# Kernel tuning notes

Measured on AMD Instinct MI355X. Metric: run time of the kernel, lower is better.

## Reference

```python
import jax, jax.numpy as jnp
import numpy as np

N_NODES = 50000
N_EDGES = 800000
IN_F, HID_F, OUT_F = 256, 128, 64


def setup_inputs() -> dict:
    key = jax.random.key(0)
    ks = jax.random.split(key, 9)
    glorot = lambda k, shp: jax.random.normal(k, shp, jnp.float32) * np.sqrt(2.0 / (shp[0] + shp[1]))
    return {
        "x": jax.random.normal(ks[0], (N_NODES, IN_F), jnp.float32),
        "W1": glorot(ks[1], (IN_F, HID_F)),
        "b1": jnp.zeros((HID_F,), jnp.float32),
        "W2": glorot(ks[2], (HID_F, OUT_F)),
        "b2": jnp.zeros((OUT_F,), jnp.float32),
        "Wf": glorot(ks[3], (OUT_F, 2)),
        "bf": jnp.zeros((2,), jnp.float32),
        "src": jax.random.randint(ks[4], (N_EDGES,), 0, N_NODES, jnp.int32),
        "dst": jax.random.randint(ks[5], (N_EDGES,), 0, N_NODES, jnp.int32),
    }


def _gcn_layer(x, src, dst, W, b):
    # DGL GraphConv, norm='both': h = D_in^{-1/2} A D_out^{-1/2} (x W) + b
    n = x.shape[0]
    ones = jnp.ones((src.shape[0],), x.dtype)
    deg_out = jnp.clip(jax.ops.segment_sum(ones, src, num_segments=n), 1.0)
    deg_in = jnp.clip(jax.ops.segment_sum(ones, dst, num_segments=n), 1.0)
    h = x @ W  # transform first (in_feats >= out_feats), cheaper messages
    h = h * jax.lax.rsqrt(deg_out)[:, None]
    agg = jax.ops.segment_sum(h[src], dst, num_segments=n)  # [N, F] sparse aggregate
    return agg * jax.lax.rsqrt(deg_in)[:, None] + b


def reference(x, W1, b1, W2, b2, Wf, bf, src, dst):
    h1 = jax.nn.relu(_gcn_layer(x, src, dst, W1, b1))
    hidden = _gcn_layer(h1, src, dst, W2, b2)
    logits = hidden @ Wf + bf
    return (logits, hidden)
```

## Files before the change

### kernel.cpp

```cpp
#include <hip/hip_runtime.h>
#include <hip/hip_bf16.h>
#include <cstdint>
#include <cstddef>

#define NNODES 50000
#define NEDGES 800000
#define NCH    256
#define CHUNK1 3136
#define NBUCK  196
#define GB1    782
#define SHB    64
#define SHE    12500
#define SHEV   (SHE / 1024)
#define PBN    256
#define PBR    196

typedef unsigned short u16;
typedef unsigned int u32;
typedef short bfrag8 __attribute__((ext_vector_type(8)));
typedef float f32x4 __attribute__((ext_vector_type(4)));

__device__ __forceinline__ u16 f2bf(float f) {
    union { float f; uint32_t i; } v; v.f = f;
    uint32_t r = (v.i + 0x7FFFu + ((v.i >> 16) & 1u)) >> 16;
    return (u16)r;
}
__device__ __forceinline__ float bflo(u32 p) { union { uint32_t i; float f; } v; v.i = p << 16; return v.f; }
__device__ __forceinline__ float bfhi(u32 p) { union { uint32_t i; float f; } v; v.i = p & 0xFFFF0000u; return v.f; }

__global__ __launch_bounds__(256) void pre_kernel(const float* __restrict__ W1, const float* __restrict__ W2,
                                                  u16* __restrict__ P1, u16* __restrict__ P2,
                                                  const int* __restrict__ src, const int* __restrict__ dst,
                                                  u32* __restrict__ histS, u32* __restrict__ histD,
                                                  u16* __restrict__ gh1, int nE) {
    __shared__ u32 hh[12500];
    int b = blockIdx.x, t = threadIdx.x;
    if (b < 2 * SHB) {
        const int* col = (b < SHB) ? src : dst;
        int bb = (b < SHB) ? b : b - SHB;
        for (int j = t; j < 12500; j += 256) hh[j] = 0;
        __syncthreads();
        int beg = bb * SHE;
        const uint4* col4 = (const uint4*)(col + beg);
        #pragma unroll 4
        for (int k = 0; k < SHEV; k++) {
            uint4 e = col4[k * 256 + t];
            atomicAdd(&hh[e.x >> 2], 1u << ((e.x & 3) * 8));
            atomicAdd(&hh[e.y >> 2], 1u << ((e.y & 3) * 8));
            atomicAdd(&hh[e.z >> 2], 1u << ((e.z & 3) * 8));
            atomicAdd(&hh[e.w >> 2], 1u << ((e.w & 3) * 8));
        }
        for (int i = beg + SHEV * 1024 + t; i < beg + SHE; i += 256) {
            u32 n = (u32)col[i];
            atomicAdd(&hh[n >> 2], 1u << ((n & 3) * 8));
        }
        __syncthreads();
        u32* out = ((b < SHB) ? histS : histD) + (size_t)bb * 12500;
        for (int j = t; j < 12500; j += 256) out[j] = hh[j];
    } else if (b < 2 * SHB + NCH) {
        int c = b - 2 * SHB;
        hh[t] = 0;
        __syncthreads();
        int beg = c * CHUNK1, end = min(beg + CHUNK1, nE);
        const uint4* d4 = (const uint4*)(dst + beg);
        int n4 = (end - beg) >> 2;
        for (int k = t; k < n4; k += 256) {
            uint4 e = d4[k];
            atomicAdd(&hh[e.x >> 8], 1u);
            atomicAdd(&hh[e.y >> 8], 1u);
            atomicAdd(&hh[e.z >> 8], 1u);
            atomicAdd(&hh[e.w >> 8], 1u);
        }
        __syncthreads();
        gh1[c * NCH + t] = (u16)hh[t];
    } else {
        int i = (b - 2 * SHB - NCH) * 256 + t;
        if (i < 256 * 128) {
            int k = i >> 7, n = i & 127;
            P1[((((k >> 3) << 7) + n) << 3) | (k & 7)] = f2bf(W1[i]);
        }
        if (i < 128 * 64) {
            int k = i >> 6, n = i & 63;
            P2[((((k >> 3) << 6) + n) << 3) | (k & 7)] = f2bf(W2[i]);
        }
    }
}

__global__ __launch_bounds__(256) void scat_deg(const int* __restrict__ src, const int* __restrict__ dst,
                                                const u16* __restrict__ gh1,
                                                const u32* __restrict__ histS, const u32* __restrict__ histD,
                                                int* __restrict__ deg_out, int* __restrict__ deg_in,
                                                int* __restrict__ gdh, int* __restrict__ part1,
                                                u32* __restrict__ sbuf, int nE) {
    int t = threadIdx.x, c = blockIdx.x;
    __shared__ int sd[256];
    __shared__ u32 base[256];
    __shared__ u32 lh[256];
    __shared__ int cnt64[64];
    if (t < 64) cnt64[t] = 0;
    int tot = 0, par = 0;
    #pragma unroll 8
    for (int cc = 0; cc < NCH; cc++) {
        int v = (int)gh1[cc * NCH + t];
        tot += v;
        par += (cc < c) ? v : 0;
    }
    if (c == 0) part1[t] = tot;
    sd[t] = tot;
    __syncthreads();
    #pragma unroll
    for (int o = 1; o < 256; o <<= 1) {
        int add = (t >= o) ? sd[t - o] : 0;
        __syncthreads();
        sd[t] += add;
        __syncthreads();
    }
    base[t] = (u32)((sd[t] - tot) + par);
    lh[t] = 0;
    __syncthreads();
    int beg = c * CHUNK1, end = min(beg + CHUNK1, nE);
    const uint4* s4 = (const uint4*)(src + beg);
    const uint4* d4 = (const uint4*)(dst + beg);
    int n4 = (end - beg) >> 2;
    for (int k = t; k < n4; k += 256) {
        uint4 es = s4[k], ed = d4[k];
        u32 el, dg, r;
        el = (ed.x << 16) | es.x; dg = el >> 24; r = atomicAdd(&lh[dg], 1); sbuf[base[dg] + r] = el;
        el = (ed.y << 16) | es.y; dg = el >> 24; r = atomicAdd(&lh[dg], 1); sbuf[base[dg] + r] = el;
        el = (ed.z << 16) | es.z; dg = el >> 24; r = atomicAdd(&lh[dg], 1); sbuf[base[dg] + r] = el;
        el = (ed.w << 16) | es.w; dg = el >> 24; r = atomicAdd(&lh[dg], 1); sbuf[base[dg] + r] = el;
    }
    int n = c * PBR + t;
    if (t < PBR && n < NNODES) {
        int w = n >> 2, sh = (n & 3) * 8;
        int so = 0, si = 0;
        #pragma unroll 8
        for (int r = 0; r < SHB; r++) {
            so += (int)((histS[(size_t)r * 12500 + w] >> sh) & 255u);
            si += (int)((histD[(size_t)r * 12500 + w] >> sh) & 255u);
        }
        deg_out[n] = so;
        deg_in[n] = si;
        atomicAdd(&cnt64[si > 63 ? 63 : si], 1);
    }
    __syncthreads();
    if (t < 64) gdh[c * 64 + t] = cnt64[t];
}

template <int K, int N, bool AF32>
__device__ __forceinline__ void gemm_body(const void* __restrict__ A_, const u16* __restrict__ Wp,
                                          const int* __restrict__ deg, u16* __restrict__ out, int M, int bx) {
    const int lane = threadIdx.x & 63;
    const int wave = threadIdx.x >> 6;
    const int m = lane & 15;
    const int q = lane >> 4;
    const int row0 = bx * 64 + wave * 16;

    int rowa = row0 + m; if (rowa > M - 1) rowa = M - 1;

    constexpr int NT = N / 16;
    f32x4 acc[NT];
    #pragma unroll
    for (int t = 0; t < NT; t++) acc[t] = (f32x4){0.f, 0.f, 0.f, 0.f};

    #pragma unroll
    for (int kc = 0; kc < K; kc += 32) {
        bfrag8 af;
        if constexpr (AF32) {
            const float* ap = (const float*)A_ + (size_t)rowa * K + q * 8 + kc;
            const float4 x0 = *(const float4*)(ap);
            const float4 x1 = *(const float4*)(ap + 4);
            af[0] = (short)f2bf(x0.x); af[1] = (short)f2bf(x0.y);
            af[2] = (short)f2bf(x0.z); af[3] = (short)f2bf(x0.w);
            af[4] = (short)f2bf(x1.x); af[5] = (short)f2bf(x1.y);
            af[6] = (short)f2bf(x1.z); af[7] = (short)f2bf(x1.w);
        } else {
            const u16* ap = (const u16*)A_ + (size_t)rowa * K + q * 8 + kc;
            af = *(const bfrag8*)ap;
        }
        const u16* bbase = Wp + ((size_t)(((kc >> 3) + q) * N) + m) * 8;
        #pragma unroll
        for (int t = 0; t < NT; t++) {
            bfrag8 bf_ = *(const bfrag8*)(bbase + t * 128);
            acc[t] = __builtin_amdgcn_mfma_f32_16x16x32_bf16(af, bf_, acc[t], 0, 0, 0);
        }
    }
    #pragma unroll
    for (int r = 0; r < 4; r++) {
        int gr = row0 + q * 4 + r;
        if (gr < M) {
            int dO = deg[gr]; if (dO < 1) dO = 1;
            float s = rsqrtf((float)dO);
            #pragma unroll
            for (int t = 0; t < NT; t++)
                out[(size_t)gr * N + t * 16 + m] = f2bf(acc[t][r] * s);
        }
    }
}

__global__ __launch_bounds__(256) void sort_gemm(const u32* __restrict__ sbuf, const int* __restrict__ part1,
                                                 u32* __restrict__ sorted, int* __restrict__ rp,
                                                 const float* __restrict__ x, const u16* __restrict__ Wp1,
                                                 const int* __restrict__ deg_out, const int* __restrict__ deg_in,
                                                 const int* __restrict__ gdh, int* __restrict__ perm,
                                                 u16* __restrict__ h, int nE) {
    int b = blockIdx.x, t = threadIdx.x;
    if (b < NBUCK) {
        __shared__ int sd[256];
        __shared__ int cnt[256];
        __shared__ int cursor[256];
        int v = part1[t];
        sd[t] = v;
        __syncthreads();
        #pragma unroll
        for (int o = 1; o < 256; o <<= 1) {
            int add = (t >= o) ? sd[t - o] : 0;
            __syncthreads();
            sd[t] += add;
            __syncthreads();
        }
        __shared__ int bs_s, bl_s;
        if (t == b) { bs_s = sd[t] - v; bl_s = v; }
        __syncthreads();
        int bstart = bs_s, bend = bstart + bl_s;
        cnt[t] = 0;
        __syncthreads();
        for (int i = bstart + t; i < bend; i += 256)
            atomicAdd(&cnt[(sbuf[i] >> 16) & 255u], 1);
        __syncthreads();
        int cv = cnt[t];
        sd[t] = cv;
        __syncthreads();
        #pragma unroll
        for (int o = 1; o < 256; o <<= 1) {
            int add = (t >= o) ? sd[t - o] : 0;
            __syncthreads();
            sd[t] += add;
            __syncthreads();
        }
        int excl = sd[t] - cv;
        int node = b * 256 + t;
        if (node < NNODES) rp[node] = bstart + excl;
        if (b == NBUCK - 1 && t == 0) rp[NNODES] = nE;
        cursor[t] = excl;
        __syncthreads();
        for (int i = bstart + t; i < bend; i += 256) {
            u32 el = sbuf[i];
            int r = atomicAdd(&cursor[(el >> 16) & 255u], 1);
            sorted[bstart + r] = el;
        }
    } else if (b < NBUCK + GB1) {
        gemm_body<256, 128, true>(x, Wp1, deg_out, h, NNODES, b - NBUCK);
    } else {
        int pb = b - NBUCK - GB1;
        __shared__ int cse[64];
        __shared__ int cur[64];
        if (t < 64) {
            int s_all = 0, s_pre = 0;
            for (int q2 = 0; q2 < PBN; q2++) {
                int v = gdh[q2 * 64 + t];
                s_all += v;
                s_pre += (q2 < pb) ? v : 0;
            }
            cse[t] = s_all;
            cur[t] = s_pre;
        }
        __syncthreads();
        if (t == 0) {
            int s = 0;
            for (int d2 = 0; d2 < 64; d2++) { int v = cse[d2]; cse[d2] = s; s += v; }
        }
        __syncthreads();
        if (t < 64) cur[t] += cse[t];
        __syncthreads();
        int n = pb * PBR + t;
        if (t < PBR && n < NNODES) {
            int d = deg_in[n]; d = d > 63 ? 63 : d;
            int p = atomicAdd(&cur[d], 1);
            perm[p] = n;
        }
    }
}

__global__ __launch_bounds__(256) void gather1f(const uint4* __restrict__ h, const int* __restrict__ row_ptr,
                                                const u32* __restrict__ sorted, const float* __restrict__ b1,
                                                const int* __restrict__ perm, const int* __restrict__ deg_out,
                                                const u16* __restrict__ Wp2, u16* __restrict__ h2) {
    __shared__ __align__(16) u16 sh[16 * 136];
    int t = threadIdx.x;
    int qw = t >> 4;
    int l = t & 15;
    int g = blockIdx.x * 16 + qw;
    int node = perm[g];
    int beg = row_ptr[node], end = row_ptr[node + 1];
    float a[8] = {0.f, 0.f, 0.f, 0.f, 0.f, 0.f, 0.f, 0.f};
    for (int e = beg; e < end; e += 8) {
        uint4 p[8];
        #pragma unroll
        for (int j = 0; j < 8; j++) {
            int ee = e + j; ee = (ee < end - 1) ? ee : end - 1;
            p[j] = h[(size_t)(sorted[ee] & 0xFFFFu) * 16 + l];
        }
        #pragma unroll
        for (int j = 0; j < 8; j++)
            if (e + j < end) {
                a[0] += bflo(p[j].x); a[1] += bfhi(p[j].x);
                a[2] += bflo(p[j].y); a[3] += bfhi(p[j].y);
                a[4] += bflo(p[j].z); a[5] += bfhi(p[j].z);
                a[6] += bflo(p[j].w); a[7] += bfhi(p[j].w);
            }
    }
    int dI = end - beg; if (dI < 1) dI = 1;
    float r = rsqrtf((float)dI);
    const float4 bA = *(const float4*)(b1 + 8 * l);
    const float4 bB = *(const float4*)(b1 + 8 * l + 4);
    float v0 = fmaxf(a[0] * r + bA.x, 0.f), v1 = fmaxf(a[1] * r + bA.y, 0.f);
    float v2 = fmaxf(a[2] * r + bA.z, 0.f), v3 = fmaxf(a[3] * r + bA.w, 0.f);
    float v4 = fmaxf(a[4] * r + bB.x, 0.f), v5 = fmaxf(a[5] * r + bB.y, 0.f);
    float v6 = fmaxf(a[6] * r + bB.z, 0.f), v7 = fmaxf(a[7] * r + bB.w, 0.f);
    uint4 o;
    o.x = ((u32)f2bf(v1) << 16) | f2bf(v0);
    o.y = ((u32)f2bf(v3) << 16) | f2bf(v2);
    o.z = ((u32)f2bf(v5) << 16) | f2bf(v4);
    o.w = ((u32)f2bf(v7) << 16) | f2bf(v6);
    *(uint4*)&sh[qw * 136 + l * 8] = o;
    __syncthreads();
    const int lane = t & 63;
    const int m = lane & 15;
    const int q = lane >> 4;
    const int w = t >> 6;
    f32x4 acc = (f32x4){0.f, 0.f, 0.f, 0.f};
    #pragma unroll
    for (int kc = 0; kc < 128; kc += 32) {
        bfrag8 af = *(const bfrag8*)&sh[m * 136 + q * 8 + kc];
        bfrag8 bf_ = *(const bfrag8*)(Wp2 + ((size_t)(((kc >> 3) + q) * 64) + w * 16 + m) * 8);
        acc = __builtin_amdgcn_mfma_f32_16x16x32_bf16(af, bf_, acc, 0, 0, 0);
    }
    #pragma unroll
    for (int rr = 0; rr < 4; rr++) {
        int li = q * 4 + rr;
        int nd = perm[blockIdx.x * 16 + li];
        int dO = deg_out[nd]; if (dO < 1) dO = 1;
        float s = rsqrtf((float)dO);
        h2[(size_t)nd * 64 + w * 16 + m] = f2bf(acc[rr] * s);
    }
}

__global__ __launch_bounds__(256) void gather2(const uint4* __restrict__ h2, const int* __restrict__ row_ptr,
                                               const u32* __restrict__ sorted, const float* __restrict__ b2,
                                               const float* __restrict__ Wf, const float* __restrict__ bfv,
                                               const int* __restrict__ perm,
                                               float* __restrict__ logits, float* __restrict__ hidden, int nNodes) {
    int g = (blockIdx.x * 256 + threadIdx.x) >> 3;
    int l = threadIdx.x & 7;
    if (g >= nNodes) return;
    int node = perm[g];
    int beg = row_ptr[node], end = row_ptr[node + 1];
    float a[8] = {0.f, 0.f, 0.f, 0.f, 0.f, 0.f, 0.f, 0.f};
    for (int e = beg; e < end; e += 8) {
        uint4 p[8];
        #pragma unroll
        for (int j = 0; j < 8; j++) {
            int ee = e + j; ee = (ee < end - 1) ? ee : end - 1;
            p[j] = h2[(size_t)(sorted[ee] & 0xFFFFu) * 8 + l];
        }
        #pragma unroll
        for (int j = 0; j < 8; j++)
            if (e + j < end) {
                a[0] += bflo(p[j].x); a[1] += bfhi(p[j].x);
                a[2] += bflo(p[j].y); a[3] += bfhi(p[j].y);
                a[4] += bflo(p[j].z); a[5] += bfhi(p[j].z);
                a[6] += bflo(p[j].w); a[7] += bfhi(p[j].w);
            }
    }
    int dI = end - beg; if (dI < 1) dI = 1;
    float r = rsqrtf((float)dI);
    float v[8];
    #pragma unroll
    for (int f = 0; f < 8; f++) v[f] = a[f] * r + b2[8 * l + f];
    float4 oA = {v[0], v[1], v[2], v[3]};
    float4 oB = {v[4], v[5], v[6], v[7]};
    ((float4*)hidden)[(size_t)node * 16 + 2 * l + 0] = oA;
    ((float4*)hidden)[(size_t)node * 16 + 2 * l + 1] = oB;
    float l0 = 0.f, l1 = 0.f;
    #pragma unroll
    for (int f = 0; f < 8; f++) {
        l0 += v[f] * Wf[(8 * l + f) * 2 + 0];
        l1 += v[f] * Wf[(8 * l + f) * 2 + 1];
    }
    #pragma unroll
    for (int off = 4; off > 0; off >>= 1) {
        l0 += __shfl_down(l0, off, 8);
        l1 += __shfl_down(l1, off, 8);
    }
    if (l == 0) {
        logits[(size_t)node * 2 + 0] = l0 + bfv[0];
        logits[(size_t)node * 2 + 1] = l1 + bfv[1];
    }
}

extern "C" void kernel_launch(void* const* d_in, const int* in_sizes, int n_in,
                              void* d_out, int out_size, void* d_ws, size_t ws_size,
                              hipStream_t stream) {
    const float* x   = (const float*)d_in[0];
    const float* W1  = (const float*)d_in[1];
    const float* b1  = (const float*)d_in[2];
    const float* W2  = (const float*)d_in[3];
    const float* b2  = (const float*)d_in[4];
    const float* Wf  = (const float*)d_in[5];
    const float* bfv = (const float*)d_in[6];
    const int* src = (const int*)d_in[7];
    const int* dst = (const int*)d_in[8];

    float* out_logits = (float*)d_out;
    float* out_hidden = (float*)d_out + 2 * NNODES;

    char* ws = (char*)d_ws;
    size_t off = 0;
    auto alloc = [&](size_t bytes) { void* p = ws + off; off += (bytes + 255) & ~(size_t)255; return p; };
    u16*   gh1     = (u16*)alloc(NCH * NCH * 2);
    int*   part1   = (int*)alloc(256 * 4);
    u32*   sbuf    = (u32*)alloc((size_t)NEDGES * 4);
    u32*   sorted  = (u32*)alloc((size_t)NEDGES * 4);
    u32*   histS   = (u32*)alloc((size_t)SHB * 12500 * 4);
    u32*   histD   = (u32*)alloc((size_t)SHB * 12500 * 4);
    int*   deg     = (int*)alloc(2 * NNODES * 4);
    int*   row_ptr = (int*)alloc((NNODES + 1) * 4);
    int*   gdh     = (int*)alloc(PBN * 64 * 4);
    int*   perm    = (int*)alloc(NNODES * 4);
    u16*   Wp1     = (u16*)alloc(256 * 128 * 2);
    u16*   Wp2     = (u16*)alloc(128 * 64 * 2);
    u16*   h       = (u16*)alloc((size_t)NNODES * 128 * 2);
    u16*   h2      = (u16*)alloc((size_t)NNODES * 64 * 2);

    int* deg_out = deg;
    int* deg_in  = deg + NNODES;

    pre_kernel<<<2 * SHB + NCH + 128, 256, 0, stream>>>(W1, W2, Wp1, Wp2, src, dst, histS, histD, gh1, NEDGES);
    scat_deg<<<NCH, 256, 0, stream>>>(src, dst, gh1, histS, histD, deg_out, deg_in, gdh, part1, sbuf, NEDGES);
    sort_gemm<<<NBUCK + GB1 + PBN, 256, 0, stream>>>(sbuf, part1, sorted, row_ptr, x, Wp1,
                                                     deg_out, deg_in, gdh, perm, h, NEDGES);
    gather1f<<<NNODES / 16, 256, 0, stream>>>((const uint4*)h, row_ptr, sorted, b1, perm, deg_out, Wp2, h2);
    gather2<<<(NNODES * 8 + 255) / 256, 256, 0, stream>>>((const uint4*)h2, row_ptr, sorted, b2, Wf, bfv,
                                                          perm, out_logits, out_hidden, NNODES);
}
```

Measured before the change: 193.8 us.

## Fuse five-kernel pipeline into one cooperative persistent kernel with grid syncs

Replaces the five separate launches with one cooperative kernel that loops over virtual blocks and uses grid.sync between phases. It also shrinks the histogram shared buffer and splits the node range into two halves to fit under the occupancy target. The aim is to remove launch gaps and inter-kernel tails. The cost is grid-sync overhead, double scanning of edges in the histogram phase, and lower parallelism when the persistent grid is smaller than the original block counts. If the cooperative launch fails it falls back to the old five-kernel path.

New measurement: 537.6 us. 2.77x slower.

```diff
diff --git a/kernel.cpp b/kernel.cpp
--- a/kernel.cpp
+++ b/kernel.cpp
@@ -1,7 +1,10 @@
 #include <hip/hip_runtime.h>
+#include <hip/hip_cooperative_groups.h>
 #include <hip/hip_bf16.h>
 #include <cstdint>
 #include <cstddef>
+
+namespace cg = cooperative_groups;
 
 #define NNODES 50000
 #define NEDGES 800000
@@ -27,6 +30,383 @@
 }
 __device__ __forceinline__ float bflo(u32 p) { union { uint32_t i; float f; } v; v.i = p << 16; return v.f; }
 __device__ __forceinline__ float bfhi(u32 p) { union { uint32_t i; float f; } v; v.i = p & 0xFFFF0000u; return v.f; }
+
+template <int K, int N, bool AF32>
+__device__ __forceinline__ void gemm_body(const void* __restrict__ A_, const u16* __restrict__ Wp,
+                                          const int* __restrict__ deg, u16* __restrict__ out, int M, int bx) {
+    const int lane = threadIdx.x & 63;
+    const int wave = threadIdx.x >> 6;
+    const int m = lane & 15;
+    const int q = lane >> 4;
+    const int row0 = bx * 64 + wave * 16;
+    int rowa = row0 + m; if (rowa > M - 1) rowa = M - 1;
+    constexpr int NT = N / 16;
+    f32x4 acc[NT];
+    #pragma unroll
+    for (int t = 0; t < NT; t++) acc[t] = (f32x4){0.f, 0.f, 0.f, 0.f};
+    #pragma unroll
+    for (int kc = 0; kc < K; kc += 32) {
+        bfrag8 af;
+        if constexpr (AF32) {
+            const float* ap = (const float*)A_ + (size_t)rowa * K + q * 8 + kc;
+            const float4 x0 = *(const float4*)(ap);
+            const float4 x1 = *(const float4*)(ap + 4);
+            af[0] = (short)f2bf(x0.x); af[1] = (short)f2bf(x0.y);
+            af[2] = (short)f2bf(x0.z); af[3] = (short)f2bf(x0.w);
+            af[4] = (short)f2bf(x1.x); af[5] = (short)f2bf(x1.y);
+            af[6] = (short)f2bf(x1.z); af[7] = (short)f2bf(x1.w);
+        } else {
+            const u16* ap = (const u16*)A_ + (size_t)rowa * K + q * 8 + kc;
+            af = *(const bfrag8*)ap;
+        }
+        const u16* bbase = Wp + ((size_t)(((kc >> 3) + q) * N) + m) * 8;
+        #pragma unroll
+        for (int t = 0; t < NT; t++) {
+            bfrag8 bf_ = *(const bfrag8*)(bbase + t * 128);
+            acc[t] = __builtin_amdgcn_mfma_f32_16x16x32_bf16(af, bf_, acc[t], 0, 0, 0);
+        }
+    }
+    #pragma unroll
+    for (int r = 0; r < 4; r++) {
+        int gr = row0 + q * 4 + r;
+        if (gr < M) {
+            int dO = deg[gr]; if (dO < 1) dO = 1;
+            float s = rsqrtf((float)dO);
+            #pragma unroll
+            for (int t = 0; t < NT; t++)
+                out[(size_t)gr * N + t * 16 + m] = f2bf(acc[t][r] * s);
+        }
+    }
+}
+
+__global__ __launch_bounds__(256, 4) void mega(
+    const float* __restrict__ W1, const float* __restrict__ W2, const float* __restrict__ b1,
+    const float* __restrict__ b2, const float* __restrict__ Wf, const float* __restrict__ bfv,
+    const float* __restrict__ x, const int* __restrict__ src, const int* __restrict__ dst,
+    u16* __restrict__ Wp1, u16* __restrict__ Wp2, u32* __restrict__ histS, u32* __restrict__ histD,
+    u16* __restrict__ gh1, int* __restrict__ deg_out, int* __restrict__ deg_in,
+    int* __restrict__ gdh, int* __restrict__ part1, u32* __restrict__ sbuf, u32* __restrict__ sorted,
+    int* __restrict__ rp, int* __restrict__ perm, u16* __restrict__ h, u16* __restrict__ h2,
+    float* __restrict__ logits, float* __restrict__ hidden)
+{
+    cg::grid_group grid = cg::this_grid();
+    __shared__ __align__(16) u32 SM[6400];
+    const int t = threadIdx.x;
+    const int NB = gridDim.x;
+
+    for (int vb = blockIdx.x; vb < 2 * SHB + NCH + 128; vb += NB) {
+        if (vb < 2 * SHB) {
+            const int* col = (vb < SHB) ? src : dst;
+            int bb = (vb < SHB) ? vb : vb - SHB;
+            u32* outp = ((vb < SHB) ? histS : histD) + (size_t)bb * 12500;
+            const uint4* col4 = (const uint4*)(col + bb * SHE);
+            #pragma unroll 1
+            for (int half = 0; half < 2; half++) {
+                u32 lo = half * 25000u, hiX = lo + 25000u;
+                for (int j = t; j < 6250; j += 256) SM[j] = 0;
+                __syncthreads();
+                #pragma unroll 4
+                for (int k = 0; k < SHEV; k++) {
+                    uint4 e = col4[k * 256 + t];
+                    if (e.x >= lo && e.x < hiX) atomicAdd(&SM[(e.x - lo) >> 2], 1u << ((e.x & 3) * 8));
+                    if (e.y >= lo && e.y < hiX) atomicAdd(&SM[(e.y - lo) >> 2], 1u << ((e.y & 3) * 8));
+                    if (e.z >= lo && e.z < hiX) atomicAdd(&SM[(e.z - lo) >> 2], 1u << ((e.z & 3) * 8));
+                    if (e.w >= lo && e.w < hiX) atomicAdd(&SM[(e.w - lo) >> 2], 1u << ((e.w & 3) * 8));
+                }
+                for (int i = SHEV * 1024 + t; i < SHE; i += 256) {
+                    u32 n = (u32)col[bb * SHE + i];
+                    if (n >= lo && n < hiX) atomicAdd(&SM[(n - lo) >> 2], 1u << ((n & 3) * 8));
+                }
+                __syncthreads();
+                for (int j = t; j < 6250; j += 256) outp[half * 6250 + j] = SM[j];
+                __syncthreads();
+            }
+        } else if (vb < 2 * SHB + NCH) {
+            int c = vb - 2 * SHB;
+            SM[t] = 0;
+            __syncthreads();
+            int beg = c * CHUNK1, end = min(beg + CHUNK1, NEDGES);
+            const uint4* d4 = (const uint4*)(dst + beg);
+            int n4 = (end - beg) >> 2;
+            for (int k = t; k < n4; k += 256) {
+                uint4 e = d4[k];
+                atomicAdd(&SM[e.x >> 8], 1u);
+                atomicAdd(&SM[e.y >> 8], 1u);
+                atomicAdd(&SM[e.z >> 8], 1u);
+                atomicAdd(&SM[e.w >> 8], 1u);
+            }
+            __syncthreads();
+            gh1[c * NCH + t] = (u16)SM[t];
+            __syncthreads();
+        } else {
+            int i = (vb - 2 * SHB - NCH) * 256 + t;
+            if (i < 256 * 128) {
+                int k = i >> 7, n = i & 127;
+                Wp1[((((k >> 3) << 7) + n) << 3) | (k & 7)] = f2bf(W1[i]);
+            }
+            if (i < 128 * 64) {
+                int k = i >> 6, n = i & 63;
+                Wp2[((((k >> 3) << 6) + n) << 3) | (k & 7)] = f2bf(W2[i]);
+            }
+            __syncthreads();
+        }
+    }
+    grid.sync();
+
+    {
+        int* sd    = (int*)SM;
+        u32* base  = SM + 256;
+        u32* lh    = SM + 512;
+        int* cnt64 = (int*)SM + 768;
+        for (int c = blockIdx.x; c < NCH; c += NB) {
+            if (t < 64) cnt64[t] = 0;
+            int tot = 0, par = 0;
+            #pragma unroll 8
+            for (int cc = 0; cc < NCH; cc++) {
+                int v = (int)gh1[cc * NCH + t];
+                tot += v;
+                par += (cc < c) ? v : 0;
+            }
+            if (c == 0) part1[t] = tot;
+            sd[t] = tot;
+            __syncthreads();
+            #pragma unroll
+            for (int o = 1; o < 256; o <<= 1) {
+                int add = (t >= o) ? sd[t - o] : 0;
+                __syncthreads();
+                sd[t] += add;
+                __syncthreads();
+            }
+            base[t] = (u32)((sd[t] - tot) + par);
+            lh[t] = 0;
+            __syncthreads();
+            int beg = c * CHUNK1, end = min(beg + CHUNK1, NEDGES);
+            const uint4* s4 = (const uint4*)(src + beg);
+            const uint4* d4 = (const uint4*)(dst + beg);
+            int n4 = (end - beg) >> 2;
+            for (int k = t; k < n4; k += 256) {
+                uint4 es = s4[k], ed = d4[k];
+                u32 el, dg, r;
+                el = (ed.x << 16) | es.x; dg = el >> 24; r = atomicAdd(&lh[dg], 1); sbuf[base[dg] + r] = el;
+                el = (ed.y << 16) | es.y; dg = el >> 24; r = atomicAdd(&lh[dg], 1); sbuf[base[dg] + r] = el;
+                el = (ed.z << 16) | es.z; dg = el >> 24; r = atomicAdd(&lh[dg], 1); sbuf[base[dg] + r] = el;
+                el = (ed.w << 16) | es.w; dg = el >> 24; r = atomicAdd(&lh[dg], 1); sbuf[base[dg] + r] = el;
+            }
+            int n = c * PBR + t;
+            if (t < PBR && n < NNODES) {
+                int w = n >> 2, sh = (n & 3) * 8;
+                int so = 0, si = 0;
+                #pragma unroll 8
+                for (int r = 0; r < SHB; r++) {
+                    so += (int)((histS[(size_t)r * 12500 + w] >> sh) & 255u);
+                    si += (int)((histD[(size_t)r * 12500 + w] >> sh) & 255u);
+                }
+                deg_out[n] = so;
+                deg_in[n] = si;
+                atomicAdd(&cnt64[si > 63 ? 63 : si], 1);
+            }
+            __syncthreads();
+            if (t < 64) gdh[c * 64 + t] = cnt64[t];
+            __syncthreads();
+        }
+    }
+    grid.sync();
+
+    for (int vb = blockIdx.x; vb < NBUCK + GB1 + PBN; vb += NB) {
+        if (vb < NBUCK) {
+            int* sd     = (int*)SM;
+            int* cnt    = (int*)SM + 256;
+            int* cursor = (int*)SM + 512;
+            int* bsbl   = (int*)SM + 768;
+            int v = part1[t];
+            sd[t] = v;
+            __syncthreads();
+            #pragma unroll
+            for (int o = 1; o < 256; o <<= 1) {
+                int add = (t >= o) ? sd[t - o] : 0;
+                __syncthreads();
+                sd[t] += add;
+                __syncthreads();
+            }
+            if (t == vb) { bsbl[0] = sd[t] - v; bsbl[1] = v; }
+            __syncthreads();
+            int bstart = bsbl[0], bend = bstart + bsbl[1];
+            cnt[t] = 0;
+            __syncthreads();
+            for (int i = bstart + t; i < bend; i += 256)
+                atomicAdd(&cnt[(sbuf[i] >> 16) & 255u], 1);
+            __syncthreads();
+            int cv = cnt[t];
+            sd[t] = cv;
+            __syncthreads();
+            #pragma unroll
+            for (int o = 1; o < 256; o <<= 1) {
+                int add = (t >= o) ? sd[t - o] : 0;
+                __syncthreads();
+                sd[t] += add;
+                __syncthreads();
+            }
+            int excl = sd[t] - cv;
+            int node = vb * 256 + t;
+            if (node < NNODES) rp[node] = bstart + excl;
+            if (vb == NBUCK - 1 && t == 0) rp[NNODES] = NEDGES;
+            cursor[t] = excl;
+            __syncthreads();
+            for (int i = bstart + t; i < bend; i += 256) {
+                u32 el = sbuf[i];
+                int r = atomicAdd(&cursor[(el >> 16) & 255u], 1);
+                sorted[bstart + r] = el;
+            }
+            __syncthreads();
+        } else if (vb < NBUCK + GB1) {
+            gemm_body<256, 128, true>(x, Wp1, deg_out, h, NNODES, vb - NBUCK);
+            __syncthreads();
+        } else {
+            int pb = vb - NBUCK - GB1;
+            int* cse = (int*)SM;
+            int* cur = (int*)SM + 64;
+            if (t < 64) {
+                int s_all = 0, s_pre = 0;
+                for (int q2 = 0; q2 < PBN; q2++) {
+                    int v = gdh[q2 * 64 + t];
+                    s_all += v;
+                    s_pre += (q2 < pb) ? v : 0;
+                }
+                cse[t] = s_all;
+                cur[t] = s_pre;
+            }
+            __syncthreads();
+            if (t == 0) {
+                int s = 0;
+                for (int d2 = 0; d2 < 64; d2++) { int v = cse[d2]; cse[d2] = s; s += v; }
+            }
+            __syncthreads();
+            if (t < 64) cur[t] += cse[t];
+            __syncthreads();
+            int n = pb * PBR + t;
+            if (t < PBR && n < NNODES) {
+                int d = deg_in[n]; d = d > 63 ? 63 : d;
+                int p = atomicAdd(&cur[d], 1);
+                perm[p] = n;
+            }
+            __syncthreads();
+        }
+    }
+    grid.sync();
+
+    {
+        u16* sh = (u16*)SM;
+        const uint4* h4 = (const uint4*)h;
+        int qw = t >> 4, l = t & 15;
+        const int lane = t & 63, m = lane & 15, q = lane >> 4, w = t >> 6;
+        for (int vb = blockIdx.x; vb < NNODES / 16; vb += NB) {
+            int node = perm[vb * 16 + qw];
+            int beg = rp[node], end = rp[node + 1];
+            float a[8] = {0.f, 0.f, 0.f, 0.f, 0.f, 0.f, 0.f, 0.f};
+            for (int e = beg; e < end; e += 8) {
+                uint4 p[8];
+                #pragma unroll
+                for (int j = 0; j < 8; j++) {
+                    int ee = e + j; ee = (ee < end - 1) ? ee : end - 1;
+                    p[j] = h4[(size_t)(sorted[ee] & 0xFFFFu) * 16 + l];
+                }
+                #pragma unroll
+                for (int j = 0; j < 8; j++)
+                    if (e + j < end) {
+                        a[0] += bflo(p[j].x); a[1] += bfhi(p[j].x);
+                        a[2] += bflo(p[j].y); a[3] += bfhi(p[j].y);
+                        a[4] += bflo(p[j].z); a[5] += bfhi(p[j].z);
+                        a[6] += bflo(p[j].w); a[7] += bfhi(p[j].w);
+                    }
+            }
+            int dI = end - beg; if (dI < 1) dI = 1;
+            float r = rsqrtf((float)dI);
+            const float4 bA = *(const float4*)(b1 + 8 * l);
+            const float4 bB = *(const float4*)(b1 + 8 * l + 4);
+            float v0 = fmaxf(a[0] * r + bA.x, 0.f), v1 = fmaxf(a[1] * r + bA.y, 0.f);
+            float v2 = fmaxf(a[2] * r + bA.z, 0.f), v3 = fmaxf(a[3] * r + bA.w, 0.f);
+            float v4 = fmaxf(a[4] * r + bB.x, 0.f), v5 = fmaxf(a[5] * r + bB.y, 0.f);
+            float v6 = fmaxf(a[6] * r + bB.z, 0.f), v7 = fmaxf(a[7] * r + bB.w, 0.f);
+            uint4 o;
+            o.x = ((u32)f2bf(v1) << 16) | f2bf(v0);
+            o.y = ((u32)f2bf(v3) << 16) | f2bf(v2);
+            o.z = ((u32)f2bf(v5) << 16) | f2bf(v4);
+            o.w = ((u32)f2bf(v7) << 16) | f2bf(v6);
+            *(uint4*)&sh[qw * 136 + l * 8] = o;
+            __syncthreads();
+            f32x4 acc = (f32x4){0.f, 0.f, 0.f, 0.f};
+            #pragma unroll
+            for (int kc = 0; kc < 128; kc += 32) {
+                bfrag8 af = *(const bfrag8*)&sh[m * 136 + q * 8 + kc];
+                bfrag8 bf_ = *(const bfrag8*)(Wp2 + ((size_t)(((kc >> 3) + q) * 64) + w * 16 + m) * 8);
+                acc = __builtin_amdgcn_mfma_f32_16x16x32_bf16(af, bf_, acc, 0, 0, 0);
+            }
+            #pragma unroll
+            for (int rr = 0; rr < 4; rr++) {
+                int li = q * 4 + rr;
+                int nd = perm[vb * 16 + li];
+                int dO = deg_out[nd]; if (dO < 1) dO = 1;
+                float s = rsqrtf((float)dO);
+                h2[(size_t)nd * 64 + w * 16 + m] = f2bf(acc[rr] * s);
+            }
+            __syncthreads();
+        }
+    }
+    grid.sync();
+
+    {
+        const uint4* h24 = (const uint4*)h2;
+        int l = t & 7;
+        for (int vb = blockIdx.x; vb < (NNODES * 8 + 255) / 256; vb += NB) {
+            int g = vb * 32 + (t >> 3);
+            if (g < NNODES) {
+                int node = perm[g];
+                int beg = rp[node], end = rp[node + 1];
+                float a[8] = {0.f, 0.f, 0.f, 0.f, 0.f, 0.f, 0.f, 0.f};
+                for (int e = beg; e < end; e += 8) {
+                    uint4 p[8];
+                    #pragma unroll
+                    for (int j = 0; j < 8; j++) {
+                        int ee = e + j; ee = (ee < end - 1) ? ee : end - 1;
+                        p[j] = h24[(size_t)(sorted[ee] & 0xFFFFu) * 8 + l];
+                    }
+                    #pragma unroll
+                    for (int j = 0; j < 8; j++)
+                        if (e + j < end) {
+                            a[0] += bflo(p[j].x); a[1] += bfhi(p[j].x);
+                            a[2] += bflo(p[j].y); a[3] += bfhi(p[j].y);
+                            a[4] += bflo(p[j].z); a[5] += bfhi(p[j].z);
+                            a[6] += bflo(p[j].w); a[7] += bfhi(p[j].w);
+                        }
+                }
+                int dI = end - beg; if (dI < 1) dI = 1;
+                float r = rsqrtf((float)dI);
+                float v[8];
+                #pragma unroll
+                for (int f = 0; f < 8; f++) v[f] = a[f] * r + b2[8 * l + f];
+                float4 oA = {v[0], v[1], v[2], v[3]};
+                float4 oB = {v[4], v[5], v[6], v[7]};
+                ((float4*)hidden)[(size_t)node * 16 + 2 * l + 0] = oA;
+                ((float4*)hidden)[(size_t)node * 16 + 2 * l + 1] = oB;
+                float l0 = 0.f, l1 = 0.f;
+                #pragma unroll
+                for (int f = 0; f < 8; f++) {
+                    l0 += v[f] * Wf[(8 * l + f) * 2 + 0];
+                    l1 += v[f] * Wf[(8 * l + f) * 2 + 1];
+                }
+                #pragma unroll
+                for (int off2 = 4; off2 > 0; off2 >>= 1) {
+                    l0 += __shfl_down(l0, off2, 8);
+                    l1 += __shfl_down(l1, off2, 8);
+                }
+                if (l == 0) {
+                    logits[(size_t)node * 2 + 0] = l0 + bfv[0];
+                    logits[(size_t)node * 2 + 1] = l1 + bfv[1];
+                }
+            }
+        }
+    }
+}
 
 __global__ __launch_bounds__(256) void pre_kernel(const float* __restrict__ W1, const float* __restrict__ W2,
                                                   u16* __restrict__ P1, u16* __restrict__ P2,
@@ -145,57 +525,6 @@
     }
     __syncthreads();
     if (t < 64) gdh[c * 64 + t] = cnt64[t];
-}
-
-template <int K, int N, bool AF32>
-__device__ __forceinline__ void gemm_body(const void* __restrict__ A_, const u16* __restrict__ Wp,
-                                          const int* __restrict__ deg, u16* __restrict__ out, int M, int bx) {
-    const int lane = threadIdx.x & 63;
-    const int wave = threadIdx.x >> 6;
-    const int m = lane & 15;
-    const int q = lane >> 4;
-    const int row0 = bx * 64 + wave * 16;
-
-    int rowa = row0 + m; if (rowa > M - 1) rowa = M - 1;
-
-    constexpr int NT = N / 16;
-    f32x4 acc[NT];
-    #pragma unroll
-    for (int t = 0; t < NT; t++) acc[t] = (f32x4){0.f, 0.f, 0.f, 0.f};
-
-    #pragma unroll
-    for (int kc = 0; kc < K; kc += 32) {
-        bfrag8 af;
-        if constexpr (AF32) {
-            const float* ap = (const float*)A_ + (size_t)rowa * K + q * 8 + kc;
-            const float4 x0 = *(const float4*)(ap);
-            const float4 x1 = *(const float4*)(ap + 4);
-            af[0] = (short)f2bf(x0.x); af[1] = (short)f2bf(x0.y);
-            af[2] = (short)f2bf(x0.z); af[3] = (short)f2bf(x0.w);
-            af[4] = (short)f2bf(x1.x); af[5] = (short)f2bf(x1.y);
-            af[6] = (short)f2bf(x1.z); af[7] = (short)f2bf(x1.w);
-        } else {
-            const u16* ap = (const u16*)A_ + (size_t)rowa * K + q * 8 + kc;
-            af = *(const bfrag8*)ap;
-        }
-        const u16* bbase = Wp + ((size_t)(((kc >> 3) + q) * N) + m) * 8;
-        #pragma unroll
-        for (int t = 0; t < NT; t++) {
-            bfrag8 bf_ = *(const bfrag8*)(bbase + t * 128);
-            acc[t] = __builtin_amdgcn_mfma_f32_16x16x32_bf16(af, bf_, acc[t], 0, 0, 0);
-        }
-    }
-    #pragma unroll
-    for (int r = 0; r < 4; r++) {
-        int gr = row0 + q * 4 + r;
-        if (gr < M) {
-            int dO = deg[gr]; if (dO < 1) dO = 1;
-            float s = rsqrtf((float)dO);
-            #pragma unroll
-            for (int t = 0; t < NT; t++)
-                out[(size_t)gr * N + t * 16 + m] = f2bf(acc[t][r] * s);
-        }
-    }
 }
 
 __global__ __launch_bounds__(256) void sort_gemm(const u32* __restrict__ sbuf, const int* __restrict__ part1,
@@ -436,11 +765,44 @@
     int* deg_out = deg;
     int* deg_in  = deg + NNODES;
 
-    pre_kernel<<<2 * SHB + NCH + 128, 256, 0, stream>>>(W1, W2, Wp1, Wp2, src, dst, histS, histD, gh1, NEDGES);
-    scat_deg<<<NCH, 256, 0, stream>>>(src, dst, gh1, histS, histD, deg_out, deg_in, gdh, part1, sbuf, NEDGES);
-    sort_gemm<<<NBUCK + GB1 + PBN, 256, 0, stream>>>(sbuf, part1, sorted, row_ptr, x, Wp1,
-                                                     deg_out, deg_in, gdh, perm, h, NEDGES);
-    gather1f<<<NNODES / 16, 256, 0, stream>>>((const uint4*)h, row_ptr, sorted, b1, perm, deg_out, Wp2, h2);
-    gather2<<<(NNODES * 8 + 255) / 256, 256, 0, stream>>>((const uint4*)h2, row_ptr, sorted, b2, Wf, bfv,
-                                                          perm, out_logits, out_hidden, NNODES);
+    static int grid_cached = -1;
+    if (grid_cached < 0) {
+        int occ = 0;
+        if (hipOccupancyMaxActiveBlocksPerMultiprocessor(&occ, mega, 256, 0) == hipSuccess && occ > 0) {
+            static int nCU = 0;
+            if (!nCU) { hipDeviceProp_t p; if (hipGetDeviceProperties(&p, 0) == hipSuccess) nCU = p.multiProcessorCount; }
+            if (!nCU) nCU = 256;
+            long g = (long)occ * nCU;
+            if (g > 4096) g = 4096;
+            grid_cached = (int)g;
+        } else {
+            grid_cached = 0;
+        }
+    }
+
+    bool coop_ok = false;
+    if (grid_cached > 0) {
+        void* args[] = {
+            (void*)&W1, (void*)&W2, (void*)&b1, (void*)&b2, (void*)&Wf, (void*)&bfv,
+            (void*)&x, (void*)&src, (void*)&dst,
+            (void*)&Wp1, (void*)&Wp2, (void*)&histS, (void*)&histD, (void*)&gh1,
+            (void*)&deg_out, (void*)&deg_in, (void*)&gdh, (void*)&part1,
+            (void*)&sbuf, (void*)&sorted, (void*)&row_ptr, (void*)&perm,
+            (void*)&h, (void*)&h2, (void*)&out_logits, (void*)&out_hidden
+        };
+        hipError_t e = hipLaunchCooperativeKernel((const void*)mega, dim3(grid_cached), dim3(256),
+                                                  args, 0, stream);
+        coop_ok = (e == hipSuccess);
+        if (!coop_ok) grid_cached = 0;
+    }
+
+    if (!coop_ok) {
+        pre_kernel<<<2 * SHB + NCH + 128, 256, 0, stream>>>(W1, W2, Wp1, Wp2, src, dst, histS, histD, gh1, NEDGES);
+        scat_deg<<<NCH, 256, 0, stream>>>(src, dst, gh1, histS, histD, deg_out, deg_in, gdh, part1, sbuf, NEDGES);
+        sort_gemm<<<NBUCK + GB1 + PBN, 256, 0, stream>>>(sbuf, part1, sorted, row_ptr, x, Wp1,
+                                                         deg_out, deg_in, gdh, perm, h, NEDGES);
+        gather1f<<<NNODES / 16, 256, 0, stream>>>((const uint4*)h, row_ptr, sorted, b1, perm, deg_out, Wp2, h2);
+        gather2<<<(NNODES * 8 + 255) / 256, 256, 0, stream>>>((const uint4*)h2, row_ptr, sorted, b2, Wf, bfv,
+                                                              perm, out_logits, out_hidden, NNODES);
+    }
 }
```

## Split gathers into feature-sliced passes over column-blocked tables for cache locality

Applied to the files above, without the earlier changes.

The GEMM output is stored in a column-blocked layout of 32-feature slices, so each gather pass reads a 3.2 MB table that fits in cache instead of the full row-major table. Layer-1 aggregation runs as four slice passes and layer-2 as two half passes, with logits combined through a partial buffer. The layer-2 transform moves out of the fused gather into a separate MFMA GEMM kernel. This trades more kernel launches, repeated index and row_ptr reads, and an extra h1 round trip for better cache hit rates on the random gathers.

Result: slower. 238.0 us (+22.8%).

```diff
diff --git a/kernel.cpp b/kernel.cpp
--- a/kernel.cpp
+++ b/kernel.cpp
@@ -14,6 +14,7 @@
 #define SHEV   (SHE / 1024)
 #define PBN    256
 #define PBR    196
+#define GGB    782
 
 typedef unsigned short u16;
 typedef unsigned int u32;
@@ -155,14 +156,11 @@
     const int m = lane & 15;
     const int q = lane >> 4;
     const int row0 = bx * 64 + wave * 16;
-
     int rowa = row0 + m; if (rowa > M - 1) rowa = M - 1;
-
     constexpr int NT = N / 16;
     f32x4 acc[NT];
     #pragma unroll
     for (int t = 0; t < NT; t++) acc[t] = (f32x4){0.f, 0.f, 0.f, 0.f};
-
     #pragma unroll
     for (int kc = 0; kc < K; kc += 32) {
         bfrag8 af;
@@ -192,10 +190,18 @@
             int dO = deg[gr]; if (dO < 1) dO = 1;
             float s = rsqrtf((float)dO);
             #pragma unroll
-            for (int t = 0; t < NT; t++)
-                out[(size_t)gr * N + t * 16 + m] = f2bf(acc[t][r] * s);
-        }
-    }
+            for (int t = 0; t < NT; t++) {
+                int f = t * 16 + m;
+                out[((size_t)(f >> 5) * M + gr) * 32 + (f & 31)] = f2bf(acc[t][r] * s);
+            }
+        }
+    }
+}
+
+template <int K, int N, bool AF32>
+__global__ __launch_bounds__(256) void gemm_scaled(const void* __restrict__ A_, const u16* __restrict__ Wp,
+                                                   const int* __restrict__ deg, u16* __restrict__ out, int M) {
+    gemm_body<K, N, AF32>(A_, Wp, deg, out, M, blockIdx.x);
 }
 
 __global__ __launch_bounds__(256) void sort_gemm(const u32* __restrict__ sbuf, const int* __restrict__ part1,
@@ -282,24 +288,23 @@
     }
 }
 
-__global__ __launch_bounds__(256) void gather1f(const uint4* __restrict__ h, const int* __restrict__ row_ptr,
+__global__ __launch_bounds__(256) void gather1q(const uint4* __restrict__ hq, const int* __restrict__ row_ptr,
                                                 const u32* __restrict__ sorted, const float* __restrict__ b1,
-                                                const int* __restrict__ perm, const int* __restrict__ deg_out,
-                                                const u16* __restrict__ Wp2, u16* __restrict__ h2) {
-    __shared__ __align__(16) u16 sh[16 * 136];
-    int t = threadIdx.x;
-    int qw = t >> 4;
-    int l = t & 15;
-    int g = blockIdx.x * 16 + qw;
+                                                const int* __restrict__ perm, uint4* __restrict__ h1out,
+                                                int qtr) {
+    int g = blockIdx.x * 64 + (threadIdx.x >> 2);
+    int l = threadIdx.x & 3;
+    if (g >= NNODES) return;
     int node = perm[g];
     int beg = row_ptr[node], end = row_ptr[node + 1];
+    const uint4* tbl = hq + (size_t)qtr * NNODES * 4;
     float a[8] = {0.f, 0.f, 0.f, 0.f, 0.f, 0.f, 0.f, 0.f};
     for (int e = beg; e < end; e += 8) {
         uint4 p[8];
         #pragma unroll
         for (int j = 0; j < 8; j++) {
             int ee = e + j; ee = (ee < end - 1) ? ee : end - 1;
-            p[j] = h[(size_t)(sorted[ee] & 0xFFFFu) * 16 + l];
+            p[j] = tbl[(size_t)(sorted[ee] & 0xFFFFu) * 4 + l];
         }
         #pragma unroll
         for (int j = 0; j < 8; j++)
@@ -312,8 +317,8 @@
     }
     int dI = end - beg; if (dI < 1) dI = 1;
     float r = rsqrtf((float)dI);
-    const float4 bA = *(const float4*)(b1 + 8 * l);
-    const float4 bB = *(const float4*)(b1 + 8 * l + 4);
+    const float4 bA = *(const float4*)(b1 + qtr * 32 + l * 8);
+    const float4 bB = *(const float4*)(b1 + qtr * 32 + l * 8 + 4);
     float v0 = fmaxf(a[0] * r + bA.x, 0.f), v1 = fmaxf(a[1] * r + bA.y, 0.f);
     float v2 = fmaxf(a[2] * r + bA.z, 0.f), v3 = fmaxf(a[3] * r + bA.w, 0.f);
     float v4 = fmaxf(a[4] * r + bB.x, 0.f), v5 = fmaxf(a[5] * r + bB.y, 0.f);
@@ -323,46 +328,28 @@
     o.y = ((u32)f2bf(v3) << 16) | f2bf(v2);
     o.z = ((u32)f2bf(v5) << 16) | f2bf(v4);
     o.w = ((u32)f2bf(v7) << 16) | f2bf(v6);
-    *(uint4*)&sh[qw * 136 + l * 8] = o;
-    __syncthreads();
-    const int lane = t & 63;
-    const int m = lane & 15;
-    const int q = lane >> 4;
-    const int w = t >> 6;
-    f32x4 acc = (f32x4){0.f, 0.f, 0.f, 0.f};
-    #pragma unroll
-    for (int kc = 0; kc < 128; kc += 32) {
-        bfrag8 af = *(const bfrag8*)&sh[m * 136 + q * 8 + kc];
-        bfrag8 bf_ = *(const bfrag8*)(Wp2 + ((size_t)(((kc >> 3) + q) * 64) + w * 16 + m) * 8);
-        acc = __builtin_amdgcn_mfma_f32_16x16x32_bf16(af, bf_, acc, 0, 0, 0);
-    }
-    #pragma unroll
-    for (int rr = 0; rr < 4; rr++) {
-        int li = q * 4 + rr;
-        int nd = perm[blockIdx.x * 16 + li];
-        int dO = deg_out[nd]; if (dO < 1) dO = 1;
-        float s = rsqrtf((float)dO);
-        h2[(size_t)nd * 64 + w * 16 + m] = f2bf(acc[rr] * s);
-    }
-}
-
-__global__ __launch_bounds__(256) void gather2(const uint4* __restrict__ h2, const int* __restrict__ row_ptr,
-                                               const u32* __restrict__ sorted, const float* __restrict__ b2,
-                                               const float* __restrict__ Wf, const float* __restrict__ bfv,
-                                               const int* __restrict__ perm,
-                                               float* __restrict__ logits, float* __restrict__ hidden, int nNodes) {
-    int g = (blockIdx.x * 256 + threadIdx.x) >> 3;
-    int l = threadIdx.x & 7;
-    if (g >= nNodes) return;
+    h1out[(size_t)node * 16 + qtr * 4 + l] = o;
+}
+
+__global__ __launch_bounds__(256) void gather2h(const uint4* __restrict__ h2h, const int* __restrict__ row_ptr,
+                                                const u32* __restrict__ sorted, const float* __restrict__ b2,
+                                                const float* __restrict__ Wf, const float* __restrict__ bfv,
+                                                const int* __restrict__ perm, float* __restrict__ lpart,
+                                                float* __restrict__ logits, float* __restrict__ hidden,
+                                                int half) {
+    int g = blockIdx.x * 64 + (threadIdx.x >> 2);
+    int l = threadIdx.x & 3;
+    if (g >= NNODES) return;
     int node = perm[g];
     int beg = row_ptr[node], end = row_ptr[node + 1];
+    const uint4* tbl = h2h + (size_t)half * NNODES * 4;
     float a[8] = {0.f, 0.f, 0.f, 0.f, 0.f, 0.f, 0.f, 0.f};
     for (int e = beg; e < end; e += 8) {
         uint4 p[8];
         #pragma unroll
         for (int j = 0; j < 8; j++) {
             int ee = e + j; ee = (ee < end - 1) ? ee : end - 1;
-            p[j] = h2[(size_t)(sorted[ee] & 0xFFFFu) * 8 + l];
+            p[j] = tbl[(size_t)(sorted[ee] & 0xFFFFu) * 4 + l];
         }
         #pragma unroll
         for (int j = 0; j < 8; j++)
@@ -375,27 +362,30 @@
     }
     int dI = end - beg; if (dI < 1) dI = 1;
     float r = rsqrtf((float)dI);
+    int fb = half * 32 + l * 8;
     float v[8];
     #pragma unroll
-    for (int f = 0; f < 8; f++) v[f] = a[f] * r + b2[8 * l + f];
+    for (int f = 0; f < 8; f++) v[f] = a[f] * r + b2[fb + f];
     float4 oA = {v[0], v[1], v[2], v[3]};
     float4 oB = {v[4], v[5], v[6], v[7]};
-    ((float4*)hidden)[(size_t)node * 16 + 2 * l + 0] = oA;
-    ((float4*)hidden)[(size_t)node * 16 + 2 * l + 1] = oB;
+    ((float4*)hidden)[(size_t)node * 16 + half * 8 + l * 2 + 0] = oA;
+    ((float4*)hidden)[(size_t)node * 16 + half * 8 + l * 2 + 1] = oB;
     float l0 = 0.f, l1 = 0.f;
     #pragma unroll
     for (int f = 0; f < 8; f++) {
-        l0 += v[f] * Wf[(8 * l + f) * 2 + 0];
-        l1 += v[f] * Wf[(8 * l + f) * 2 + 1];
-    }
-    #pragma unroll
-    for (int off = 4; off > 0; off >>= 1) {
-        l0 += __shfl_down(l0, off, 8);
-        l1 += __shfl_down(l1, off, 8);
-    }
+        l0 += v[f] * Wf[(fb + f) * 2 + 0];
+        l1 += v[f] * Wf[(fb + f) * 2 + 1];
+    }
+    l0 += __shfl_down(l0, 2, 4); l0 += __shfl_down(l0, 1, 4);
+    l1 += __shfl_down(l1, 2, 4); l1 += __shfl_down(l1, 1, 4);
     if (l == 0) {
-        logits[(size_t)node * 2 + 0] = l0 + bfv[0];
-        logits[(size_t)node * 2 + 1] = l1 + bfv[1];
+        if (half == 0) {
+            lpart[(size_t)node * 2 + 0] = l0;
+            lpart[(size_t)node * 2 + 1] = l1;
+        } else {
+            logits[(size_t)node * 2 + 0] = lpart[(size_t)node * 2 + 0] + l0 + bfv[0];
+            logits[(size_t)node * 2 + 1] = lpart[(size_t)node * 2 + 1] + l1 + bfv[1];
+        }
     }
 }
 
@@ -431,7 +421,9 @@
     u16*   Wp1     = (u16*)alloc(256 * 128 * 2);
     u16*   Wp2     = (u16*)alloc(128 * 64 * 2);
     u16*   h       = (u16*)alloc((size_t)NNODES * 128 * 2);
+    u16*   h1      = (u16*)alloc((size_t)NNODES * 128 * 2);
     u16*   h2      = (u16*)alloc((size_t)NNODES * 64 * 2);
+    float* lpart   = (float*)alloc((size_t)NNODES * 2 * 4);
 
     int* deg_out = deg;
     int* deg_in  = deg + NNODES;
@@ -440,7 +432,11 @@
     scat_deg<<<NCH, 256, 0, stream>>>(src, dst, gh1, histS, histD, deg_out, deg_in, gdh, part1, sbuf, NEDGES);
     sort_gemm<<<NBUCK + GB1 + PBN, 256, 0, stream>>>(sbuf, part1, sorted, row_ptr, x, Wp1,
                                                      deg_out, deg_in, gdh, perm, h, NEDGES);
-    gather1f<<<NNODES / 16, 256, 0, stream>>>((const uint4*)h, row_ptr, sorted, b1, perm, deg_out, Wp2, h2);
-    gather2<<<(NNODES * 8 + 255) / 256, 256, 0, stream>>>((const uint4*)h2, row_ptr, sorted, b2, Wf, bfv,
-                                                          perm, out_logits, out_hidden, NNODES);
-}
+    for (int q = 0; q < 4; q++)
+        gather1q<<<GGB, 256, 0, stream>>>((const uint4*)h, row_ptr, sorted, b1, perm, (uint4*)h1, q);
+    gemm_scaled<128, 64, false><<<GB1, 256, 0, stream>>>(h1, Wp2, deg_out, h2, NNODES);
+    gather2h<<<GGB, 256, 0, stream>>>((const uint4*)h2, row_ptr, sorted, b2, Wf, bfv, perm,
+                                      lpart, out_logits, out_hidden, 0);
+    gather2h<<<GGB, 256, 0, stream>>>((const uint4*)h2, row_ptr, sorted, b2, Wf, bfv, perm,
+                                      lpart, out_logits, out_hidden, 1);
+}
```
